# Kernel optimization log

Hardware: AMD Instinct MI355X
Metric: run time of the kernel (lower is better)

Reference implementation:

```python
import jax, jax.numpy as jnp
import numpy as np

NUM_NODES = 100_000
NUM_EDGES = 3_200_000
NUM_GRAPHS = 200
F_IN = 128
HID = 64
BN_EPS = 1e-5


def setup_inputs() -> dict:
    key = jax.random.key(0)
    ks = jax.random.split(key, 12)
    x = jax.random.normal(ks[0], (NUM_NODES, F_IN), dtype=jnp.float32)
    edge_index = jax.random.randint(ks[1], (2, NUM_EDGES), 0, NUM_NODES, dtype=jnp.int64)
    batch = jnp.sort(jax.random.randint(ks[2], (NUM_NODES,), 0, NUM_GRAPHS, dtype=jnp.int64))
    s1 = float(np.sqrt(6.0 / F_IN))  # kaiming_uniform-ish bound
    s2 = float(np.sqrt(6.0 / HID))
    W1 = jax.random.uniform(ks[3], (HID, F_IN), jnp.float32, -s1, s1)
    b1 = jnp.zeros((HID,), jnp.float32)
    W2 = jax.random.uniform(ks[4], (HID, HID), jnp.float32, -s2, s2)
    b2 = jnp.zeros((HID,), jnp.float32)
    gamma1 = jnp.ones((HID,), jnp.float32)
    beta1 = jnp.zeros((HID,), jnp.float32)
    mean1 = 0.1 * jax.random.normal(ks[5], (HID,), jnp.float32)
    var1 = jax.random.uniform(ks[6], (HID,), jnp.float32, 0.5, 1.5)
    gamma2 = jnp.ones((HID,), jnp.float32)
    beta2 = jnp.zeros((HID,), jnp.float32)
    mean2 = 0.1 * jax.random.normal(ks[7], (HID,), jnp.float32)
    var2 = jax.random.uniform(ks[8], (HID,), jnp.float32, 0.5, 1.5)
    Wl = jax.random.uniform(ks[9], (1, HID), jnp.float32, -s2, s2)
    bl = jnp.zeros((1,), jnp.float32)
    return dict(x=x, edge_index=edge_index, batch=batch,
                W1=W1, b1=b1, gamma1=gamma1, beta1=beta1, mean1=mean1, var1=var1,
                W2=W2, b2=b2, gamma2=gamma2, beta2=beta2, mean2=mean2, var2=var2,
                Wl=Wl, bl=bl)


def _gcn_conv(x, W, b, src, dst, dinv):
    # PyG GCNConv: h = x @ W.T, then D^{-1/2}(A+I)D^{-1/2} aggregation, then + bias
    h = x @ W.T                                    # [N, out]
    w_edge = (dinv[src] * dinv[dst])[:, None]      # [E, 1]
    msg = h[src] * w_edge                          # [E, out] gather
    agg = jax.ops.segment_sum(msg, dst, num_segments=NUM_NODES)
    agg = agg + h * (dinv * dinv)[:, None]         # self-loop term
    return agg + b


def _bn_eval(h, gamma, beta, mean, var):
    return (h - mean) * (gamma * jax.lax.rsqrt(var + BN_EPS)) + beta


def reference(x, edge_index, batch,
              W1, b1, gamma1, beta1, mean1, var1,
              W2, b2, gamma2, beta2, mean2, var2,
              Wl, bl):
    src, dst = edge_index[0], edge_index[1]
    # degrees over A + I (self-loops add 1)
    deg = jax.ops.segment_sum(jnp.ones((NUM_EDGES,), jnp.float32), dst,
                              num_segments=NUM_NODES) + 1.0
    dinv = jax.lax.rsqrt(deg)
    h = jax.nn.relu(_bn_eval(_gcn_conv(x, W1, b1, src, dst, dinv),
                             gamma1, beta1, mean1, var1))
    # dropout = identity (eval mode)
    h = jax.nn.relu(_bn_eval(_gcn_conv(h, W2, b2, src, dst, dinv),
                             gamma2, beta2, mean2, var2))
    # global_mean_pool over graph ids
    sums = jax.ops.segment_sum(h, batch, num_segments=NUM_GRAPHS)
    cnts = jax.ops.segment_sum(jnp.ones((NUM_NODES,), jnp.float32), batch,
                               num_segments=NUM_GRAPHS)
    pooled = sums / jnp.maximum(cnts, 1.0)[:, None]  # [G, 64]
    return pooled @ Wl.T + bl                        # [G, 1]
```

## Files before the change

### kernel.cpp

```cpp
#include <hip/hip_runtime.h>
#include <hip/hip_bf16.h>

#define NN 100000
#define FF 128
#define HH 64
#define BN_EPS 1e-5f

__global__ void k_detect(const unsigned* __restrict__ ei, int* __restrict__ flag) {
    if (threadIdx.x == 0 && blockIdx.x == 0) {
        unsigned o = 0;
        for (int i = 1; i < 32; i += 2) o |= ei[i];
        *flag = (o == 0) ? 1 : 0;
    }
}

__device__ __forceinline__ int load_idx(const void* p, int i, int is64) {
    return is64 ? (int)((const long long*)p)[i] : ((const int*)p)[i];
}

__global__ void k_count(const void* __restrict__ ei, int E, const int* __restrict__ flag,
                        int* __restrict__ counts) {
    int e = blockIdx.x * blockDim.x + threadIdx.x;
    if (e >= E) return;
    int is64 = *flag;
    int d = load_idx(ei, E + e, is64);
    atomicAdd(&counts[d], 1);
}

__global__ void k_dinv(const int* __restrict__ counts, float* __restrict__ dinv,
                       const void* __restrict__ bat, const int* __restrict__ flag,
                       int* __restrict__ gcnt, int N) {
    int i = blockIdx.x * blockDim.x + threadIdx.x;
    if (i >= N) return;
    float deg = (float)counts[i] + 1.0f;
    dinv[i] = rsqrtf(deg);
    int is64 = *flag;
    int b = load_idx(bat, i, is64);
    atomicAdd(&gcnt[b], 1);
}

__global__ void k_scan1(const int* __restrict__ counts, int* __restrict__ partial, int N) {
    __shared__ int s[512];
    int t = threadIdx.x;
    int i = blockIdx.x * 512 + t;
    int v = (i < N) ? counts[i] : 0;
    s[t] = v; __syncthreads();
    for (int off = 256; off; off >>= 1) {
        if (t < off) s[t] += s[t + off];
        __syncthreads();
    }
    if (t == 0) partial[blockIdx.x] = s[0];
}

__global__ void k_scan2(int* __restrict__ partial, int nch) {
    __shared__ int s[256];
    int t = threadIdx.x;
    int v = (t < nch) ? partial[t] : 0;
    s[t] = v; __syncthreads();
    for (int off = 1; off < 256; off <<= 1) {
        int add = (t >= off) ? s[t - off] : 0;
        __syncthreads();
        s[t] += add;
        __syncthreads();
    }
    if (t < nch) partial[t] = s[t] - v;
}

__global__ void k_scan3(const int* __restrict__ counts, const int* __restrict__ partial,
                        int* __restrict__ rp, int N, int E) {
    __shared__ int s[512];
    int t = threadIdx.x;
    int i = blockIdx.x * 512 + t;
    int v = (i < N) ? counts[i] : 0;
    s[t] = v; __syncthreads();
    for (int off = 1; off < 512; off <<= 1) {
        int add = (t >= off) ? s[t - off] : 0;
        __syncthreads();
        s[t] += add;
        __syncthreads();
    }
    if (i < N) rp[i] = partial[blockIdx.x] + s[t] - v;
    if (i == N) rp[N] = E;
}

__global__ void k_fill(const void* __restrict__ ei, int E, const int* __restrict__ flag,
                       const float* __restrict__ dinv, const int* __restrict__ rp,
                       int* __restrict__ fillcnt, int2* __restrict__ cw) {
    int e = blockIdx.x * blockDim.x + threadIdx.x;
    if (e >= E) return;
    int is64 = *flag;
    int s = load_idx(ei, e, is64);
    int d = load_idx(ei, E + e, is64);
    float w = dinv[s] * dinv[d];
    int pos = rp[d] + atomicAdd(&fillcnt[d], 1);
    int2 p; p.x = s; p.y = __float_as_int(w);
    cw[pos] = p;
}

__global__ void k_prep(const float* b1, const float* g1, const float* be1,
                       const float* m1, const float* v1,
                       const float* b2, const float* g2, const float* be2,
                       const float* m2, const float* v2,
                       float* sc1, float* sh1, float* sc2, float* sh2) {
    int f = threadIdx.x;
    if (f < HH) {
        float s1 = g1[f] * rsqrtf(v1[f] + BN_EPS);
        sc1[f] = s1; sh1[f] = (b1[f] - m1[f]) * s1 + be1[f];
        float s2 = g2[f] * rsqrtf(v2[f] + BN_EPS);
        sc2[f] = s2; sh2[f] = (b2[f] - m2[f]) * s2 + be2[f];
    }
}

template <int K, int NPB>
__global__ void k_gemm(const float* __restrict__ x, const float* __restrict__ W,
                       float* __restrict__ out, int N) {
    __shared__ float wT[K * (HH + 1)];
    __shared__ float xs[NPB * K];
    const int TB = NPB * 64;
    int t = threadIdx.x;
    for (int idx = t; idx < K * HH; idx += TB) {
        int f = idx / K, k = idx % K;
        wT[k * (HH + 1) + f] = W[idx];
    }
    int nb = blockIdx.x * NPB;
    for (int idx = t; idx < NPB * K; idx += TB) {
        int gi = nb * K + idx;
        xs[idx] = (gi < N * K) ? x[gi] : 0.0f;
    }
    __syncthreads();
    int f = t & 63, nl = t >> 6;
    float acc = 0.0f;
#pragma unroll
    for (int k = 0; k < K; k++)
        acc += xs[nl * K + k] * wT[k * (HH + 1) + f];
    int n = nb + nl;
    if (n < N) out[n * HH + f] = acc;
}

template <int LAYER>
__global__ void k_agg(const float* __restrict__ h, const int2* __restrict__ cw,
                      const int* __restrict__ rp, const float* __restrict__ dinv,
                      const float* __restrict__ sc, const float* __restrict__ sh,
                      float* __restrict__ out,
                      const void* __restrict__ bat, const int* __restrict__ flag,
                      const float* __restrict__ Wl, float* __restrict__ gsum, int N) {
    int wid = (int)((blockIdx.x * blockDim.x + threadIdx.x) >> 6);
    int f = threadIdx.x & 63;
    if (wid >= N) return;
    float di = dinv[wid];
    float acc = h[wid * HH + f] * di * di;
    int s = rp[wid], e = rp[wid + 1];
    int j = s;
    for (; j + 1 < e; j += 2) {
        int2 p0 = cw[j], p1 = cw[j + 1];
        acc += __int_as_float(p0.y) * h[p0.x * HH + f];
        acc += __int_as_float(p1.y) * h[p1.x * HH + f];
    }
    if (j < e) {
        int2 p = cw[j];
        acc += __int_as_float(p.y) * h[p.x * HH + f];
    }
    float v = fmaxf(acc * sc[f] + sh[f], 0.0f);
    if (LAYER == 1) {
        out[wid * HH + f] = v;
    } else {
        float tval = v * Wl[f];
        for (int off = 32; off; off >>= 1) tval += __shfl_down(tval, off);
        if (f == 0) {
            int is64 = *flag;
            int b = load_idx(bat, wid, is64);
            atomicAdd(&gsum[b], tval);
        }
    }
}

__global__ void k_final(const float* __restrict__ gsum, const int* __restrict__ gcnt,
                        const float* __restrict__ bl, float* __restrict__ outp, int G) {
    int g = blockIdx.x * blockDim.x + threadIdx.x;
    if (g < G) outp[g] = gsum[g] / fmaxf((float)gcnt[g], 1.0f) + bl[0];
}

extern "C" void kernel_launch(void* const* d_in, const int* in_sizes, int n_in,
                              void* d_out, int out_size, void* d_ws, size_t ws_size,
                              hipStream_t stream) {
    const float* x   = (const float*)d_in[0];
    const void*  ei  = d_in[1];
    const void*  bat = d_in[2];
    const float* W1  = (const float*)d_in[3];
    const float* b1  = (const float*)d_in[4];
    const float* g1  = (const float*)d_in[5];
    const float* be1 = (const float*)d_in[6];
    const float* m1  = (const float*)d_in[7];
    const float* v1  = (const float*)d_in[8];
    const float* W2  = (const float*)d_in[9];
    const float* b2  = (const float*)d_in[10];
    const float* g2  = (const float*)d_in[11];
    const float* be2 = (const float*)d_in[12];
    const float* m2  = (const float*)d_in[13];
    const float* v2  = (const float*)d_in[14];
    const float* Wl  = (const float*)d_in[15];
    const float* bl  = (const float*)d_in[16];
    float* outp = (float*)d_out;

    const int N = NN;
    const int E = in_sizes[1] / 2;
    const int G = out_size;

    char* base = (char*)d_ws;
    size_t off = 0;
    auto alloc = [&](size_t bytes) { void* p = base + off; off = (off + bytes + 255) & ~(size_t)255; return p; };
    int*   flag    = (int*)  alloc(16);
    float* dinv    = (float*)alloc((size_t)N * 4);
    int*   counts  = (int*)  alloc((size_t)N * 4);
    int*   rp      = (int*)  alloc(((size_t)N + 1) * 4);
    int*   fillcnt = (int*)  alloc((size_t)N * 4);
    int*   partial = (int*)  alloc(1024);
    float* sc1     = (float*)alloc(HH * 4);
    float* sh1     = (float*)alloc(HH * 4);
    float* sc2     = (float*)alloc(HH * 4);
    float* sh2     = (float*)alloc(HH * 4);
    float* gsum    = (float*)alloc((size_t)G * 4);
    int*   gcnt    = (int*)  alloc((size_t)G * 4);
    int2*  cw      = (int2*) alloc((size_t)E * 8);
    float* bufA    = (float*)alloc((size_t)N * HH * 4);
    float* bufB    = (float*)alloc((size_t)N * HH * 4);
    (void)ws_size;

    hipMemsetAsync(counts, 0, (size_t)N * 4, stream);
    hipMemsetAsync(fillcnt, 0, (size_t)N * 4, stream);
    hipMemsetAsync(gsum, 0, (size_t)G * 4, stream);
    hipMemsetAsync(gcnt, 0, (size_t)G * 4, stream);

    k_detect<<<1, 64, 0, stream>>>((const unsigned*)ei, flag);

    int eb = (E + 255) / 256;
    k_count<<<eb, 256, 0, stream>>>(ei, E, flag, counts);

    int nb = (N + 255) / 256;
    k_dinv<<<nb, 256, 0, stream>>>(counts, dinv, bat, flag, gcnt, N);

    int nch = (N + 511) / 512;
    k_scan1<<<nch, 512, 0, stream>>>(counts, partial, N);
    k_scan2<<<1, 256, 0, stream>>>(partial, nch);
    k_scan3<<<nch, 512, 0, stream>>>(counts, partial, rp, N, E);

    k_fill<<<eb, 256, 0, stream>>>(ei, E, flag, dinv, rp, fillcnt, cw);

    k_prep<<<1, 64, 0, stream>>>(b1, g1, be1, m1, v1, b2, g2, be2, m2, v2,
                                 sc1, sh1, sc2, sh2);

    k_gemm<FF, 8><<<(N + 7) / 8, 512, 0, stream>>>(x, W1, bufA, N);
    k_agg<1><<<(N + 3) / 4, 256, 0, stream>>>(bufA, cw, rp, dinv, sc1, sh1, bufB,
                                              bat, flag, Wl, gsum, N);
    k_gemm<HH, 8><<<(N + 7) / 8, 512, 0, stream>>>(bufB, W2, bufA, N);
    k_agg<2><<<(N + 3) / 4, 256, 0, stream>>>(bufA, cw, rp, dinv, sc2, sh2, nullptr,
                                              bat, flag, Wl, gsum, N);

    k_final<<<1, 256, 0, stream>>>(gsum, gcnt, bl, outp, G);
}
```

Before: 1.359 ms.

## Bucket edges by destination tile and source block for shared-memory aggregation

Replaces per-node CSR aggregation with tiles of 240 destination nodes whose edges are bucketed by 8192-node source block. Each tile accumulates into shared memory with LDS float atomics, and the sweep over source blocks is meant to keep gathered feature rows in cache. The CSR build now keys on (tile, source block), and source id plus local destination are packed into one int. The cost is many shared-memory atomics, only about 417 blocks in flight, and a larger scan.

```diff
diff --git a/kernel.cpp b/kernel.cpp
--- a/kernel.cpp
+++ b/kernel.cpp
@@ -5,6 +5,12 @@
 #define FF 128
 #define HH 64
 #define BN_EPS 1e-5f
+
+#define TILE 240
+#define NT   ((NN + TILE - 1) / TILE)
+#define SBLK 8192
+#define NBLK ((NN + SBLK - 1) / SBLK)
+#define NKEY (NT * NBLK)
 
 __global__ void k_detect(const unsigned* __restrict__ ei, int* __restrict__ flag) {
     if (threadIdx.x == 0 && blockIdx.x == 0) {
@@ -19,12 +25,15 @@
 }
 
 __global__ void k_count(const void* __restrict__ ei, int E, const int* __restrict__ flag,
-                        int* __restrict__ counts) {
+                        int* __restrict__ counts, int* __restrict__ counts2) {
     int e = blockIdx.x * blockDim.x + threadIdx.x;
     if (e >= E) return;
     int is64 = *flag;
+    int s = load_idx(ei, e, is64);
     int d = load_idx(ei, E + e, is64);
     atomicAdd(&counts[d], 1);
+    int key = (d / TILE) * NBLK + (s >> 13);
+    atomicAdd(&counts2[key], 1);
 }
 
 __global__ void k_dinv(const int* __restrict__ counts, float* __restrict__ dinv,
@@ -83,18 +92,21 @@
     if (i == N) rp[N] = E;
 }
 
-__global__ void k_fill(const void* __restrict__ ei, int E, const int* __restrict__ flag,
-                       const float* __restrict__ dinv, const int* __restrict__ rp,
-                       int* __restrict__ fillcnt, int2* __restrict__ cw) {
+__global__ void k_fill2(const void* __restrict__ ei, int E, const int* __restrict__ flag,
+                        const float* __restrict__ dinv, const int* __restrict__ rp2,
+                        int* __restrict__ fill2, int2* __restrict__ cw2) {
     int e = blockIdx.x * blockDim.x + threadIdx.x;
     if (e >= E) return;
     int is64 = *flag;
     int s = load_idx(ei, e, is64);
     int d = load_idx(ei, E + e, is64);
     float w = dinv[s] * dinv[d];
-    int pos = rp[d] + atomicAdd(&fillcnt[d], 1);
-    int2 p; p.x = s; p.y = __float_as_int(w);
-    cw[pos] = p;
+    int tile = d / TILE;
+    int key = tile * NBLK + (s >> 13);
+    int dl = d - tile * TILE;
+    int pos = rp2[key] + atomicAdd(&fill2[key], 1);
+    int2 p; p.x = s | (dl << 17); p.y = __float_as_int(w);
+    cw2[pos] = p;
 }
 
 __global__ void k_prep(const float* b1, const float* g1, const float* be1,
@@ -138,38 +150,98 @@
 }
 
 template <int LAYER>
-__global__ void k_agg(const float* __restrict__ h, const int2* __restrict__ cw,
-                      const int* __restrict__ rp, const float* __restrict__ dinv,
-                      const float* __restrict__ sc, const float* __restrict__ sh,
-                      float* __restrict__ out,
-                      const void* __restrict__ bat, const int* __restrict__ flag,
-                      const float* __restrict__ Wl, float* __restrict__ gsum, int N) {
-    int wid = (int)((blockIdx.x * blockDim.x + threadIdx.x) >> 6);
-    int f = threadIdx.x & 63;
-    if (wid >= N) return;
-    float di = dinv[wid];
-    float acc = h[wid * HH + f] * di * di;
-    int s = rp[wid], e = rp[wid + 1];
-    int j = s;
-    for (; j + 1 < e; j += 2) {
-        int2 p0 = cw[j], p1 = cw[j + 1];
-        acc += __int_as_float(p0.y) * h[p0.x * HH + f];
-        acc += __int_as_float(p1.y) * h[p1.x * HH + f];
-    }
-    if (j < e) {
-        int2 p = cw[j];
-        acc += __int_as_float(p.y) * h[p.x * HH + f];
-    }
-    float v = fmaxf(acc * sc[f] + sh[f], 0.0f);
+__global__ __launch_bounds__(256, 2) void k_agg2(
+        const float* __restrict__ h, const int2* __restrict__ cw2,
+        const int* __restrict__ rp2, const float* __restrict__ dinv,
+        const float* __restrict__ sc, const float* __restrict__ sh,
+        float* __restrict__ out, const void* __restrict__ bat,
+        const int* __restrict__ flag, const float* __restrict__ Wl,
+        float* __restrict__ gsum, int N) {
+    __shared__ float acc[TILE * 65];
+    const float4* __restrict__ h4 = (const float4*)h;
+    int tile = blockIdx.x, d0 = tile * TILE, t = threadIdx.x;
+
+    for (int idx = t; idx < TILE * 16; idx += 256) {
+        int dl = idx >> 4, fl = idx & 15, d = d0 + dl;
+        float4 v = make_float4(0.f, 0.f, 0.f, 0.f);
+        if (d < N) {
+            float di = dinv[d]; float s2 = di * di;
+            float4 r = h4[d * 16 + fl];
+            v.x = r.x * s2; v.y = r.y * s2; v.z = r.z * s2; v.w = r.w * s2;
+        }
+        int base = dl * 65 + fl * 4;
+        acc[base + 0] = v.x; acc[base + 1] = v.y;
+        acc[base + 2] = v.z; acc[base + 3] = v.w;
+    }
+    __syncthreads();
+
+    int w = t >> 6, lane = t & 63, q = lane >> 4, fl = lane & 15;
+    for (int b = 0; b < NBLK; b++) {
+        int kk = tile * NBLK + b;
+        int s0 = rp2[kk], e0 = rp2[kk + 1];
+        int len = e0 - s0;
+        int ws = s0 + ((len * w) >> 2);
+        int we = s0 + ((len * (w + 1)) >> 2);
+        for (int j = ws; j < we; j += 16) {
+            int2 p[4]; int vld[4];
+#pragma unroll
+            for (int u = 0; u < 4; u++) {
+                int jj = j + u * 4 + q;
+                vld[u] = jj < we;
+                int xi = vld[u] ? jj : (we - 1);
+                p[u] = cw2[xi];
+            }
+#pragma unroll
+            for (int u = 0; u < 4; u++) {
+                float wgt = vld[u] ? __int_as_float(p[u].y) : 0.f;
+                int src = p[u].x & 0x1FFFF;
+                int dl = p[u].x >> 17;
+                float4 r = h4[src * 16 + fl];
+                int base = dl * 65 + fl * 4;
+                atomicAdd(&acc[base + 0], wgt * r.x);
+                atomicAdd(&acc[base + 1], wgt * r.y);
+                atomicAdd(&acc[base + 2], wgt * r.z);
+                atomicAdd(&acc[base + 3], wgt * r.w);
+            }
+        }
+    }
+    __syncthreads();
+
     if (LAYER == 1) {
-        out[wid * HH + f] = v;
+        for (int idx = t; idx < TILE * 16; idx += 256) {
+            int dl = idx >> 4, f4 = idx & 15, d = d0 + dl;
+            if (d < N) {
+                int base = dl * 65 + f4 * 4; int f0 = f4 * 4;
+                float4 o;
+                o.x = fmaxf(acc[base + 0] * sc[f0 + 0] + sh[f0 + 0], 0.f);
+                o.y = fmaxf(acc[base + 1] * sc[f0 + 1] + sh[f0 + 1], 0.f);
+                o.z = fmaxf(acc[base + 2] * sc[f0 + 2] + sh[f0 + 2], 0.f);
+                o.w = fmaxf(acc[base + 3] * sc[f0 + 3] + sh[f0 + 3], 0.f);
+                ((float4*)out)[d * 16 + f4] = o;
+            }
+        }
     } else {
-        float tval = v * Wl[f];
-        for (int off = 32; off; off >>= 1) tval += __shfl_down(tval, off);
-        if (f == 0) {
-            int is64 = *flag;
-            int b = load_idx(bat, wid, is64);
-            atomicAdd(&gsum[b], tval);
+        int is64 = *flag;
+        int f4 = t & 15, f0 = f4 * 4;
+        for (int dl = (t >> 4); dl < TILE; dl += 16) {
+            int d = d0 + dl;
+            float tv = 0.f;
+            if (d < N) {
+                int base = dl * 65 + f0;
+                float a0 = fmaxf(acc[base + 0] * sc[f0 + 0] + sh[f0 + 0], 0.f);
+                float a1 = fmaxf(acc[base + 1] * sc[f0 + 1] + sh[f0 + 1], 0.f);
+                float a2 = fmaxf(acc[base + 2] * sc[f0 + 2] + sh[f0 + 2], 0.f);
+                float a3 = fmaxf(acc[base + 3] * sc[f0 + 3] + sh[f0 + 3], 0.f);
+                tv = a0 * Wl[f0] + a1 * Wl[f0 + 1] + a2 * Wl[f0 + 2] + a3 * Wl[f0 + 3];
+            }
+            tv += __shfl_xor(tv, 1);
+            tv += __shfl_xor(tv, 2);
+            tv += __shfl_xor(tv, 4);
+            tv += __shfl_xor(tv, 8);
+            if (f4 == 0 && d < N) {
+                int bg = load_idx(bat, d, is64);
+                atomicAdd(&gsum[bg], tv);
+            }
         }
     }
 }
@@ -212,49 +284,51 @@
     int*   flag    = (int*)  alloc(16);
     float* dinv    = (float*)alloc((size_t)N * 4);
     int*   counts  = (int*)  alloc((size_t)N * 4);
-    int*   rp      = (int*)  alloc(((size_t)N + 1) * 4);
-    int*   fillcnt = (int*)  alloc((size_t)N * 4);
-    int*   partial = (int*)  alloc(1024);
+    int*   counts2 = (int*)  alloc((size_t)NKEY * 4);
+    int*   fill2   = (int*)  alloc((size_t)NKEY * 4);
+    int*   rp2     = (int*)  alloc(((size_t)NKEY + 1) * 4);
+    int*   partial = (int*)  alloc(4096);
     float* sc1     = (float*)alloc(HH * 4);
     float* sh1     = (float*)alloc(HH * 4);
     float* sc2     = (float*)alloc(HH * 4);
     float* sh2     = (float*)alloc(HH * 4);
     float* gsum    = (float*)alloc((size_t)G * 4);
     int*   gcnt    = (int*)  alloc((size_t)G * 4);
-    int2*  cw      = (int2*) alloc((size_t)E * 8);
+    int2*  cw2     = (int2*) alloc((size_t)E * 8);
     float* bufA    = (float*)alloc((size_t)N * HH * 4);
     float* bufB    = (float*)alloc((size_t)N * HH * 4);
     (void)ws_size;
 
     hipMemsetAsync(counts, 0, (size_t)N * 4, stream);
-    hipMemsetAsync(fillcnt, 0, (size_t)N * 4, stream);
+    hipMemsetAsync(counts2, 0, (size_t)NKEY * 4, stream);
+    hipMemsetAsync(fill2, 0, (size_t)NKEY * 4, stream);
     hipMemsetAsync(gsum, 0, (size_t)G * 4, stream);
     hipMemsetAsync(gcnt, 0, (size_t)G * 4, stream);
 
     k_detect<<<1, 64, 0, stream>>>((const unsigned*)ei, flag);
 
     int eb = (E + 255) / 256;
-    k_count<<<eb, 256, 0, stream>>>(ei, E, flag, counts);
+    k_count<<<eb, 256, 0, stream>>>(ei, E, flag, counts, counts2);
 
     int nb = (N + 255) / 256;
     k_dinv<<<nb, 256, 0, stream>>>(counts, dinv, bat, flag, gcnt, N);
 
-    int nch = (N + 511) / 512;
-    k_scan1<<<nch, 512, 0, stream>>>(counts, partial, N);
-    k_scan2<<<1, 256, 0, stream>>>(partial, nch);
-    k_scan3<<<nch, 512, 0, stream>>>(counts, partial, rp, N, E);
-
-    k_fill<<<eb, 256, 0, stream>>>(ei, E, flag, dinv, rp, fillcnt, cw);
+    int kch = (NKEY + 511) / 512;
+    k_scan1<<<kch, 512, 0, stream>>>(counts2, partial, NKEY);
+    k_scan2<<<1, 256, 0, stream>>>(partial, kch);
+    k_scan3<<<kch, 512, 0, stream>>>(counts2, partial, rp2, NKEY, E);
+
+    k_fill2<<<eb, 256, 0, stream>>>(ei, E, flag, dinv, rp2, fill2, cw2);
 
     k_prep<<<1, 64, 0, stream>>>(b1, g1, be1, m1, v1, b2, g2, be2, m2, v2,
                                  sc1, sh1, sc2, sh2);
 
     k_gemm<FF, 8><<<(N + 7) / 8, 512, 0, stream>>>(x, W1, bufA, N);
-    k_agg<1><<<(N + 3) / 4, 256, 0, stream>>>(bufA, cw, rp, dinv, sc1, sh1, bufB,
-                                              bat, flag, Wl, gsum, N);
+    k_agg2<1><<<NT, 256, 0, stream>>>(bufA, cw2, rp2, dinv, sc1, sh1, bufB,
+                                      bat, flag, Wl, gsum, N);
     k_gemm<HH, 8><<<(N + 7) / 8, 512, 0, stream>>>(bufB, W2, bufA, N);
-    k_agg<2><<<(N + 3) / 4, 256, 0, stream>>>(bufA, cw, rp, dinv, sc2, sh2, nullptr,
-                                              bat, flag, Wl, gsum, N);
+    k_agg2<2><<<NT, 256, 0, stream>>>(bufA, cw2, rp2, dinv, sc2, sh2, nullptr,
+                                      bat, flag, Wl, gsum, N);
 
     k_final<<<1, 256, 0, stream>>>(gsum, gcnt, bl, outp, G);
 }
```

After: 3.706 ms. +172.8%, slower.
